# Performance work log

Hardware: AMD Instinct MI355X
Metric: run time of the kernel (lower is better)

The kernel has to match this reference:

```python
import jax, jax.numpy as jnp
import numpy as np

# Module constants (from init_kwargs)
N_BANDS = 15
BW = 129          # uniform bandwidth of every band
HOP = 64
N_FREQ = 1025
EMB = 128
MLP = 512
C = 2             # in_channel (stereo)
REIM = 2          # complex mask -> (real, imag)
OUT = BW * C * REIM   # 516 ; pre-GLU linear outputs 2*OUT
STARTS = np.arange(N_BANDS) * HOP  # band start bins
LN_EPS = 1e-5


def setup_inputs() -> dict:
    key = jax.random.key(0)
    ks = jax.random.split(key, 6)
    B, T = 2, 2048
    q = jax.random.normal(ks[0], (B, N_BANDS, T, EMB), jnp.float32)
    # Per-band LayerNorm affine params
    ln_gamma = jnp.ones((N_BANDS, EMB), jnp.float32)
    ln_beta = jnp.zeros((N_BANDS, EMB), jnp.float32)
    # Per-band hidden Linear (emb -> mlp) and output Linear (mlp -> 2*OUT, then GLU)
    W1 = jax.random.normal(ks[1], (N_BANDS, EMB, MLP), jnp.float32) * (1.0 / np.sqrt(EMB))
    b1 = jax.random.normal(ks[2], (N_BANDS, MLP), jnp.float32) * 0.01
    W2 = jax.random.normal(ks[3], (N_BANDS, MLP, 2 * OUT), jnp.float32) * (1.0 / np.sqrt(MLP))
    b2 = jax.random.normal(ks[4], (N_BANDS, 2 * OUT), jnp.float32) * 0.01
    # Per-band frequency weights (buffers), shape [n_bands, bandwidth]
    freq_weights = jax.random.uniform(ks[5], (N_BANDS, BW), jnp.float32, 0.1, 1.0)
    return {"q": q, "ln_gamma": ln_gamma, "ln_beta": ln_beta,
            "W1": W1, "b1": b1, "W2": W2, "b2": b2,
            "freq_weights": freq_weights}


def reference(q, ln_gamma, ln_beta, W1, b1, W2, b2, freq_weights):
    # q: [B, n_bands, T, emb]
    B, n, T, E = q.shape
    # Per-band LayerNorm over last dim
    mu = jnp.mean(q, axis=-1, keepdims=True)
    var = jnp.mean(jnp.square(q - mu), axis=-1, keepdims=True)
    qn = (q - mu) * jax.lax.rsqrt(var + LN_EPS)
    qn = qn * ln_gamma[None, :, None, :] + ln_beta[None, :, None, :]
    # hidden: Linear + Tanh (batched over bands)
    h = jnp.tanh(jnp.einsum('bnte,nef->bntf', qn, W1) + b1[None, :, None, :])
    # output: Linear + GLU(dim=-1)
    o = jnp.einsum('bntf,nfo->bnto', h, W2) + b2[None, :, None, :]
    a, g = o[..., :OUT], o[..., OUT:]
    m = a * jax.nn.sigmoid(g)                      # [B, n, T, OUT]
    # reshape_output: [B, n, T, C, BW, reim] -> (permute 0,2,3,1 per band) -> [B, C, n, BW, T, reim]
    m = m.reshape(B, n, T, C, BW, REIM)
    m = jnp.transpose(m, (0, 3, 1, 4, 2, 5))       # [B, C, n, BW, T, 2]
    # freq weighting: fw[:, None] broadcast over time
    m = m * freq_weights[None, None, :, :, None, None]
    # Overlapping scatter-add into [B, C, n_freq, T, 2]
    idx = (jnp.asarray(STARTS)[:, None] + jnp.arange(BW)[None, :]).reshape(-1)  # [n*BW]
    masks = jnp.zeros((B, C, N_FREQ, T, REIM), q.dtype)
    masks = masks.at[:, :, idx, :, :].add(m.reshape(B, C, n * BW, T, REIM))
    # Last dim (real, imag) is the real view of the complex mask.
    return masks
```

## Files before the change

kernel.cpp:

```cpp
#include <hip/hip_runtime.h>
#include <math.h>

#define NB    15
#define BWID  129
#define HOP   64
#define NFREQ 1025
#define EMB   128
#define MLP   512
#define OUTC  516
#define O2    1032
#define BATCH 2
#define TLEN  2048
#define REIM  2
#define CCH   2
#define RTOT  (BATCH*NB*TLEN)

typedef _Float16 half8 __attribute__((ext_vector_type(8)));
typedef _Float16 half4 __attribute__((ext_vector_type(4)));
typedef _Float16 half2_ __attribute__((ext_vector_type(2)));
typedef float    floatx4 __attribute__((ext_vector_type(4)));

#define GLOAD_LDS(gsrc, ldst) \
  __builtin_amdgcn_global_load_lds((const __attribute__((address_space(1))) unsigned int*)(gsrc), \
                                   (__attribute__((address_space(3))) unsigned int*)(ldst), 16, 0, 0)

__global__ __launch_bounds__(256) void ln_kernel(const float* __restrict__ q,
                                                 const float* __restrict__ gamma,
                                                 const float* __restrict__ beta,
                                                 _Float16* __restrict__ qn)
{
    int row  = blockIdx.x * 4 + (threadIdx.x >> 6);
    int lane = threadIdx.x & 63;
    int n    = (row / TLEN) % NB;

    const float2* src = (const float2*)(q + (size_t)row * EMB);
    float2 v = src[lane];
    float s  = v.x + v.y;
    float s2 = v.x * v.x + v.y * v.y;
    #pragma unroll
    for (int off = 1; off < 64; off <<= 1) {
        s  += __shfl_xor(s,  off);
        s2 += __shfl_xor(s2, off);
    }
    float mu   = s * (1.0f / EMB);
    float var  = s2 * (1.0f / EMB) - mu * mu;
    float rstd = rsqrtf(var + 1e-5f);

    float2 g2 = ((const float2*)(gamma + n * EMB))[lane];
    float2 b2 = ((const float2*)(beta  + n * EMB))[lane];
    half2_ o;
    o[0] = (_Float16)((v.x - mu) * rstd * g2.x + b2.x);
    o[1] = (_Float16)((v.y - mu) * rstd * g2.y + b2.y);
    ((half2_*)(qn + (size_t)row * EMB))[lane] = o;
}

__global__ __launch_bounds__(256) void transpose_cvt(const float* __restrict__ src,
                                                     _Float16* __restrict__ dst,
                                                     int R, int C)
{
    __shared__ float tile[32][33];
    const int band = blockIdx.z;
    src += (size_t)band * R * C;
    dst += (size_t)band * R * C;
    int tx = threadIdx.x & 31, ty = threadIdx.x >> 5;
    int c0 = blockIdx.x * 32, r0 = blockIdx.y * 32;
    int c = c0 + tx;
    if (c < C) {
        #pragma unroll
        for (int i = 0; i < 4; ++i)
            tile[ty + i * 8][tx] = src[(size_t)(r0 + ty + i * 8) * C + c];
    }
    __syncthreads();
    int cl = threadIdx.x >> 3, rq = (threadIdx.x & 7) * 4;
    int cw = c0 + cl;
    if (cw < C) {
        half4 v;
        #pragma unroll
        for (int j = 0; j < 4; ++j) v[j] = (_Float16)tile[rq + j][cl];
        *(half4*)(dst + (size_t)cw * R + r0 + rq) = v;
    }
}

__global__ __launch_bounds__(256) void gemm1_mfma(const _Float16* __restrict__ qn,
                                                  const _Float16* __restrict__ W1T,
                                                  const float* __restrict__ b1,
                                                  _Float16* __restrict__ h)
{
    __shared__ _Float16 sA[128 * 64];
    __shared__ _Float16 sB[128 * 64];
    const int n   = blockIdx.z;
    const int m0  = blockIdx.y * 128;
    const int n0  = blockIdx.x * 128;
    const int tid = threadIdx.x;
    const int lane = tid & 63;
    const int wave = tid >> 6;
    const int wr = (wave >> 1) * 64;
    const int wc = (wave & 1) * 64;
    const int b = m0 >> 11, t0 = m0 & (TLEN - 1);

    const _Float16* Ab = qn  + ((size_t)(b * NB + n) * TLEN + t0) * EMB;
    const _Float16* Bb = W1T + ((size_t)n * MLP + n0) * EMB;

    floatx4 acc[4][4] = {};

    const int lrow = lane & 15;
    const int q16  = (lane >> 4) << 4;
    const int swz  = (lane & 7) << 4;

    for (int k0 = 0; k0 < EMB; k0 += 64) {
        #pragma unroll
        for (int i = 0; i < 4; ++i) {
            int g = tid + i * 256;
            int r = g >> 3, kb = g & 7;
            int sk = kb ^ (r & 7);
            GLOAD_LDS(Ab + (size_t)r * EMB + k0 + sk * 8, sA + g * 8);
            GLOAD_LDS(Bb + (size_t)r * EMB + k0 + sk * 8, sB + g * 8);
        }
        __syncthreads();
        #pragma unroll
        for (int kk = 0; kk < 2; ++kk) {
            half8 af[4], bf[4];
            #pragma unroll
            for (int m = 0; m < 4; ++m) {
                int r = wr + m * 16 + lrow;
                af[m] = *(const half8*)((const char*)sA + r * 128 + (((kk << 6) | q16) ^ swz));
            }
            #pragma unroll
            for (int nf = 0; nf < 4; ++nf) {
                int r = wc + nf * 16 + lrow;
                bf[nf] = *(const half8*)((const char*)sB + r * 128 + (((kk << 6) | q16) ^ swz));
            }
            #pragma unroll
            for (int m = 0; m < 4; ++m)
                #pragma unroll
                for (int nf = 0; nf < 4; ++nf)
                    acc[m][nf] = __builtin_amdgcn_mfma_f32_16x16x32_f16(af[m], bf[nf], acc[m][nf], 0, 0, 0);
        }
        __syncthreads();
    }

    const int rq = (lane >> 4) * 4;
    _Float16* hb = h + ((size_t)(b * NB + n) * TLEN + t0) * MLP;
    #pragma unroll
    for (int nf = 0; nf < 4; ++nf) {
        int col = n0 + wc + nf * 16 + lrow;
        float bias = b1[n * MLP + col];
        #pragma unroll
        for (int m = 0; m < 4; ++m) {
            int rbase = wr + m * 16 + rq;
            #pragma unroll
            for (int r = 0; r < 4; ++r) {
                float v = tanhf(acc[m][nf][r] + bias);
                hb[(size_t)(rbase + r) * MLP + col] = (_Float16)v;
            }
        }
    }
}

__global__ __launch_bounds__(512) void gemm2_mfma(const _Float16* __restrict__ h,
                                                  const _Float16* __restrict__ W2T,
                                                  const float* __restrict__ b2,
                                                  const float* __restrict__ fw,
                                                  _Float16* __restrict__ mws)
{
    __shared__ _Float16 sA[3 * 256 * 64];
    __shared__ _Float16 sB[3 * 128 * 64];

    const int NWG = 9 * 16 * NB;
    int flat = blockIdx.x;
    int wg   = (flat & 7) * (NWG / 8) + (flat >> 3);
    int bx   = wg % 9;
    int tmp  = wg / 9;
    int by   = tmp & 15;
    int n    = tmp >> 4;

    const int m0  = by * 256;
    const int n0  = bx * 64;
    const int tid = threadIdx.x;
    const int lane = tid & 63;
    const int wave = tid >> 6;
    const int wm = (wave >> 1) * 64;
    const int wc = (wave & 1) * 32;
    const int b = m0 >> 11, t0 = m0 & (TLEN - 1);

    const _Float16* Ab  = h   + ((size_t)(b * NB + n) * TLEN + t0) * MLP;
    const _Float16* W2n = W2T + (size_t)n * O2 * MLP;

    floatx4 accA[4][2] = {};
    floatx4 accG[4][2] = {};

    const int lrow = lane & 15;
    const int q16  = (lane >> 4) << 4;
    const int swz  = (lane & 7) << 4;

    auto stageA2 = [&](int slot, int k0, int i0) {
        #pragma unroll
        for (int i = i0; i < i0 + 2; ++i) {
            int g = tid + i * 512;
            int r = g >> 3;
            int sk = (g & 7) ^ (r & 7);
            GLOAD_LDS(Ab + (size_t)r * MLP + k0 + sk * 8, sA + slot * 16384 + g * 8);
        }
    };
    auto stageBa = [&](int slot, int k0) {
        int g = tid, r = g >> 3;
        int sk = (g & 7) ^ (r & 7);
        int ra = n0 + r; if (ra > OUTC - 1) ra = OUTC - 1;
        GLOAD_LDS(W2n + (size_t)ra * MLP + k0 + sk * 8, sB + slot * 8192 + g * 8);
    };
    auto stageBg = [&](int slot, int k0) {
        int g = tid, r = g >> 3;
        int sk = (g & 7) ^ (r & 7);
        int rg = OUTC + n0 + r; if (rg > O2 - 1) rg = O2 - 1;
        GLOAD_LDS(W2n + (size_t)rg * MLP + k0 + sk * 8, sB + slot * 8192 + 4096 + g * 8);
    };

    stageA2(0, 0, 0);  stageBa(0, 0);
    stageA2(0, 0, 2);  stageBg(0, 0);
    stageA2(1, 64, 0); stageBa(1, 64);
    stageA2(1, 64, 2); stageBg(1, 64);

    for (int kt = 0; kt < 8; ++kt) {
        if (kt < 7) asm volatile("s_waitcnt vmcnt(6)" ::: "memory");
        else        asm volatile("s_waitcnt vmcnt(0)" ::: "memory");
        __builtin_amdgcn_sched_barrier(0);
        __builtin_amdgcn_s_barrier();
        __builtin_amdgcn_sched_barrier(0);

        const int cur = kt % 3;
        const int kt2 = kt + 2;
        const int pre = kt2 % 3;
        const int kp  = kt2 * 64;
        const bool ds = kt2 < 8;
        const _Float16* sAc = sA + cur * 16384;
        const _Float16* sBc = sB + cur * 8192;

        #pragma unroll
        for (int kk = 0; kk < 2; ++kk) {
            half8 af[4], ba[2], bg[2];
            const int koff = (kk << 6) | q16;
            #pragma unroll
            for (int m = 0; m < 4; ++m)
                af[m] = *(const half8*)((const char*)sAc + (wm + m * 16 + lrow) * 128 + (koff ^ swz));
            #pragma unroll
            for (int nf = 0; nf < 2; ++nf) {
                ba[nf] = *(const half8*)((const char*)sBc + (wc + nf * 16 + lrow) * 128 + (koff ^ swz));
                bg[nf] = *(const half8*)((const char*)sBc + 8192 + (wc + nf * 16 + lrow) * 128 + (koff ^ swz));
            }
            if (ds) {
                if (kk == 0) { stageA2(pre, kp, 0); stageBa(pre, kp); }
                else         { stageA2(pre, kp, 2); stageBg(pre, kp); }
            }
            __builtin_amdgcn_sched_barrier(0);
            __builtin_amdgcn_s_barrier();
            asm volatile("s_waitcnt lgkmcnt(0)" ::: "memory");
            __builtin_amdgcn_sched_barrier(0);
            __builtin_amdgcn_s_setprio(1);
            #pragma unroll
            for (int m = 0; m < 4; ++m)
                #pragma unroll
                for (int nf = 0; nf < 2; ++nf) {
                    accA[m][nf] = __builtin_amdgcn_mfma_f32_16x16x32_f16(af[m], ba[nf], accA[m][nf], 0, 0, 0);
                    accG[m][nf] = __builtin_amdgcn_mfma_f32_16x16x32_f16(af[m], bg[nf], accG[m][nf], 0, 0, 0);
                }
            __builtin_amdgcn_s_setprio(0);
            __builtin_amdgcn_sched_barrier(0);
            if (kk == 0) __builtin_amdgcn_s_barrier();
        }
    }

    const int rq = (lane >> 4) * 4;
    const float* b2n = b2 + n * O2;
    #pragma unroll
    for (int nf = 0; nf < 2; ++nf) {
        int c = n0 + wc + nf * 16 + lrow;
        bool valid = c < OUTC;
        int cl = valid ? c : OUTC - 1;
        float biasA = b2n[cl];
        float biasG = b2n[OUTC + cl];
        int rem = cl % 258;
        float w = fw[n * BWID + (rem >> 1)];
        _Float16* mb = mws + ((size_t)((b * NB + n) * OUTC + cl)) * TLEN + t0;
        #pragma unroll
        for (int m = 0; m < 4; ++m) {
            int tb = wm + m * 16 + rq;
            half4 vals;
            #pragma unroll
            for (int r = 0; r < 4; ++r) {
                float a = accA[m][nf][r] + biasA;
                float g = accG[m][nf][r] + biasG;
                vals[r] = (_Float16)(a * w / (1.0f + expf(-g)));
            }
            if (valid) *(half4*)(mb + tb) = vals;
        }
    }
}

__global__ __launch_bounds__(256) void gather_masks(const _Float16* __restrict__ mws,
                                                    float* __restrict__ out)
{
    const int f  = blockIdx.x;
    const int bc = blockIdx.y;
    const int b  = bc >> 1, cc = bc & 1;
    int nlo = (f >= 129) ? ((f - 65) >> 6) : 0;
    int nhi = f >> 6; if (nhi > 14) nhi = 14;
    const int t0 = threadIdx.x * 8;

    float a[8] = {0,0,0,0,0,0,0,0};
    float g[8] = {0,0,0,0,0,0,0,0};
    for (int nn = nlo; nn <= nhi; ++nn) {
        int bw = f - (nn << 6);
        int cbase = cc * 258 + (bw << 1);
        const _Float16* p = mws + ((size_t)((b * NB + nn) * OUTC + cbase)) * TLEN + t0;
        half8 va = *(const half8*)p;
        half8 vg = *(const half8*)(p + TLEN);
        #pragma unroll
        for (int j = 0; j < 8; ++j) { a[j] += (float)va[j]; g[j] += (float)vg[j]; }
    }
    float* ob = out + (((size_t)bc * NFREQ + f) * TLEN + t0) * REIM;
    #pragma unroll
    for (int j = 0; j < 4; ++j) {
        float4 v = make_float4(a[2*j], g[2*j], a[2*j+1], g[2*j+1]);
        *(float4*)(ob + j * 4) = v;
    }
}

extern "C" void kernel_launch(void* const* d_in, const int* in_sizes, int n_in,
                              void* d_out, int out_size, void* d_ws, size_t ws_size,
                              hipStream_t stream) {
    const float* q     = (const float*)d_in[0];
    const float* gamma = (const float*)d_in[1];
    const float* beta  = (const float*)d_in[2];
    const float* W1    = (const float*)d_in[3];
    const float* b1    = (const float*)d_in[4];
    const float* W2    = (const float*)d_in[5];
    const float* b2    = (const float*)d_in[6];
    const float* fw    = (const float*)d_in[7];

    _Float16* hws  = (_Float16*)d_ws;
    _Float16* mws  = hws + (size_t)RTOT * MLP;
    _Float16* qnws = mws + (size_t)BATCH * NB * OUTC * TLEN;
    _Float16* W1T  = qnws + (size_t)RTOT * EMB;
    _Float16* W2T  = qnws;

    ln_kernel<<<RTOT / 4, 256, 0, stream>>>(q, gamma, beta, qnws);
    transpose_cvt<<<dim3(16, 4, NB), 256, 0, stream>>>(W1, W1T, EMB, MLP);
    gemm1_mfma<<<dim3(4, 32, NB), 256, 0, stream>>>(qnws, W1T, b1, hws);
    transpose_cvt<<<dim3(33, 16, NB), 256, 0, stream>>>(W2, W2T, MLP, O2);
    gemm2_mfma<<<9 * 16 * NB, 512, 0, stream>>>(hws, W2T, b2, fw, mws);
    gather_masks<<<dim3(NFREQ, BATCH * CCH), 256, 0, stream>>>(mws, (float*)d_out);
}
```

Measured before the change: 313.5 us.

## Merge weight transposes, widen LayerNorm loads, simplify gemm2 to double buffering

LayerNorm now processes rows with 32 lanes each using float4 loads and half4 stores. The two weight transpose launches are merged into one, with W2T placed in its own workspace region after W1T so it no longer aliases qn. In gemm2, the triple-buffered pipeline with manual vmcnt waits and split barriers is replaced by a double buffer that syncs with __syncthreads. This cuts LDS use and may raise occupancy, but it drops the deeper prefetch and the fine-grained overlap of loads with MFMA work.

```diff
diff --git a/kernel.cpp b/kernel.cpp
--- a/kernel.cpp
+++ b/kernel.cpp
@@ -13,11 +13,10 @@
 #define TLEN  2048
 #define REIM  2
 #define CCH   2
-#define RTOT  (BATCH*NB*TLEN)
+#define RTOT  (BATCH*TLEN*NB)
 
 typedef _Float16 half8 __attribute__((ext_vector_type(8)));
 typedef _Float16 half4 __attribute__((ext_vector_type(4)));
-typedef _Float16 half2_ __attribute__((ext_vector_type(2)));
 typedef float    floatx4 __attribute__((ext_vector_type(4)));
 
 #define GLOAD_LDS(gsrc, ldst) \
@@ -29,16 +28,15 @@
                                                  const float* __restrict__ beta,
                                                  _Float16* __restrict__ qn)
 {
-    int row  = blockIdx.x * 4 + (threadIdx.x >> 6);
-    int lane = threadIdx.x & 63;
-    int n    = (row / TLEN) % NB;
-
-    const float2* src = (const float2*)(q + (size_t)row * EMB);
-    float2 v = src[lane];
-    float s  = v.x + v.y;
-    float s2 = v.x * v.x + v.y * v.y;
+    int row = blockIdx.x * 8 + (threadIdx.x >> 5);
+    int l32 = threadIdx.x & 31;
+    int n   = (row / TLEN) % NB;
+
+    float4 v = ((const float4*)(q + (size_t)row * EMB))[l32];
+    float s  = v.x + v.y + v.z + v.w;
+    float s2 = v.x * v.x + v.y * v.y + v.z * v.z + v.w * v.w;
     #pragma unroll
-    for (int off = 1; off < 64; off <<= 1) {
+    for (int off = 1; off < 32; off <<= 1) {
         s  += __shfl_xor(s,  off);
         s2 += __shfl_xor(s2, off);
     }
@@ -46,24 +44,36 @@
     float var  = s2 * (1.0f / EMB) - mu * mu;
     float rstd = rsqrtf(var + 1e-5f);
 
-    float2 g2 = ((const float2*)(gamma + n * EMB))[lane];
-    float2 b2 = ((const float2*)(beta  + n * EMB))[lane];
-    half2_ o;
-    o[0] = (_Float16)((v.x - mu) * rstd * g2.x + b2.x);
-    o[1] = (_Float16)((v.y - mu) * rstd * g2.y + b2.y);
-    ((half2_*)(qn + (size_t)row * EMB))[lane] = o;
-}
-
-__global__ __launch_bounds__(256) void transpose_cvt(const float* __restrict__ src,
-                                                     _Float16* __restrict__ dst,
-                                                     int R, int C)
+    float4 g4 = ((const float4*)(gamma + n * EMB))[l32];
+    float4 b4 = ((const float4*)(beta  + n * EMB))[l32];
+    half4 o;
+    o[0] = (_Float16)((v.x - mu) * rstd * g4.x + b4.x);
+    o[1] = (_Float16)((v.y - mu) * rstd * g4.y + b4.y);
+    o[2] = (_Float16)((v.z - mu) * rstd * g4.z + b4.z);
+    o[3] = (_Float16)((v.w - mu) * rstd * g4.w + b4.w);
+    ((half4*)(qn + (size_t)row * EMB))[l32] = o;
+}
+
+__global__ __launch_bounds__(256) void transpose_cvt_all(const float* __restrict__ W1,
+                                                         const float* __restrict__ W2,
+                                                         _Float16* __restrict__ W1T,
+                                                         _Float16* __restrict__ W2T)
 {
     __shared__ float tile[32][33];
-    const int band = blockIdx.z;
-    src += (size_t)band * R * C;
-    dst += (size_t)band * R * C;
+    int bid = blockIdx.x;
+    const float* src; _Float16* dst; int R, C, bx, by;
+    if (bid < 960) {
+        int band = bid >> 6; int t = bid & 63; bx = t & 15; by = t >> 4;
+        R = EMB; C = MLP;
+        src = W1 + (size_t)band * R * C; dst = W1T + (size_t)band * R * C;
+    } else {
+        int b2 = bid - 960;
+        int band = b2 / 528; int t = b2 % 528; bx = t % 33; by = t / 33;
+        R = MLP; C = O2;
+        src = W2 + (size_t)band * R * C; dst = W2T + (size_t)band * R * C;
+    }
     int tx = threadIdx.x & 31, ty = threadIdx.x >> 5;
-    int c0 = blockIdx.x * 32, r0 = blockIdx.y * 32;
+    int c0 = bx * 32, r0 = by * 32;
     int c = c0 + tx;
     if (c < C) {
         #pragma unroll
@@ -163,8 +173,8 @@
                                                   const float* __restrict__ fw,
                                                   _Float16* __restrict__ mws)
 {
-    __shared__ _Float16 sA[3 * 256 * 64];
-    __shared__ _Float16 sB[3 * 128 * 64];
+    __shared__ _Float16 sA[2 * 256 * 64];
+    __shared__ _Float16 sB[2 * 128 * 64];
 
     const int NWG = 9 * 16 * NB;
     int flat = blockIdx.x;
@@ -193,48 +203,32 @@
     const int q16  = (lane >> 4) << 4;
     const int swz  = (lane & 7) << 4;
 
-    auto stageA2 = [&](int slot, int k0, int i0) {
-        #pragma unroll
-        for (int i = i0; i < i0 + 2; ++i) {
+    auto stage = [&](int slot, int k0) {
+        #pragma unroll
+        for (int i = 0; i < 4; ++i) {
             int g = tid + i * 512;
             int r = g >> 3;
             int sk = (g & 7) ^ (r & 7);
             GLOAD_LDS(Ab + (size_t)r * MLP + k0 + sk * 8, sA + slot * 16384 + g * 8);
         }
+        {
+            int g = tid, r = g >> 3;
+            int sk = (g & 7) ^ (r & 7);
+            int ra = n0 + r;        if (ra > OUTC - 1) ra = OUTC - 1;
+            int rg = OUTC + n0 + r; if (rg > O2 - 1)   rg = O2 - 1;
+            GLOAD_LDS(W2n + (size_t)ra * MLP + k0 + sk * 8, sB + slot * 8192 + g * 8);
+            GLOAD_LDS(W2n + (size_t)rg * MLP + k0 + sk * 8, sB + slot * 8192 + 4096 + g * 8);
+        }
     };
-    auto stageBa = [&](int slot, int k0) {
-        int g = tid, r = g >> 3;
-        int sk = (g & 7) ^ (r & 7);
-        int ra = n0 + r; if (ra > OUTC - 1) ra = OUTC - 1;
-        GLOAD_LDS(W2n + (size_t)ra * MLP + k0 + sk * 8, sB + slot * 8192 + g * 8);
-    };
-    auto stageBg = [&](int slot, int k0) {
-        int g = tid, r = g >> 3;
-        int sk = (g & 7) ^ (r & 7);
-        int rg = OUTC + n0 + r; if (rg > O2 - 1) rg = O2 - 1;
-        GLOAD_LDS(W2n + (size_t)rg * MLP + k0 + sk * 8, sB + slot * 8192 + 4096 + g * 8);
-    };
-
-    stageA2(0, 0, 0);  stageBa(0, 0);
-    stageA2(0, 0, 2);  stageBg(0, 0);
-    stageA2(1, 64, 0); stageBa(1, 64);
-    stageA2(1, 64, 2); stageBg(1, 64);
+
+    stage(0, 0);
+    __syncthreads();
 
     for (int kt = 0; kt < 8; ++kt) {
-        if (kt < 7) asm volatile("s_waitcnt vmcnt(6)" ::: "memory");
-        else        asm volatile("s_waitcnt vmcnt(0)" ::: "memory");
-        __builtin_amdgcn_sched_barrier(0);
-        __builtin_amdgcn_s_barrier();
-        __builtin_amdgcn_sched_barrier(0);
-
-        const int cur = kt % 3;
-        const int kt2 = kt + 2;
-        const int pre = kt2 % 3;
-        const int kp  = kt2 * 64;
-        const bool ds = kt2 < 8;
+        const int cur = kt & 1;
+        if (kt < 7) stage(cur ^ 1, (kt + 1) * 64);
         const _Float16* sAc = sA + cur * 16384;
         const _Float16* sBc = sB + cur * 8192;
-
         #pragma unroll
         for (int kk = 0; kk < 2; ++kk) {
             half8 af[4], ba[2], bg[2];
@@ -247,14 +241,6 @@
                 ba[nf] = *(const half8*)((const char*)sBc + (wc + nf * 16 + lrow) * 128 + (koff ^ swz));
                 bg[nf] = *(const half8*)((const char*)sBc + 8192 + (wc + nf * 16 + lrow) * 128 + (koff ^ swz));
             }
-            if (ds) {
-                if (kk == 0) { stageA2(pre, kp, 0); stageBa(pre, kp); }
-                else         { stageA2(pre, kp, 2); stageBg(pre, kp); }
-            }
-            __builtin_amdgcn_sched_barrier(0);
-            __builtin_amdgcn_s_barrier();
-            asm volatile("s_waitcnt lgkmcnt(0)" ::: "memory");
-            __builtin_amdgcn_sched_barrier(0);
             __builtin_amdgcn_s_setprio(1);
             #pragma unroll
             for (int m = 0; m < 4; ++m)
@@ -264,9 +250,8 @@
                     accG[m][nf] = __builtin_amdgcn_mfma_f32_16x16x32_f16(af[m], bg[nf], accG[m][nf], 0, 0, 0);
                 }
             __builtin_amdgcn_s_setprio(0);
-            __builtin_amdgcn_sched_barrier(0);
-            if (kk == 0) __builtin_amdgcn_s_barrier();
-        }
+        }
+        __syncthreads();
     }
 
     const int rq = (lane >> 4) * 4;
@@ -341,12 +326,11 @@
     _Float16* mws  = hws + (size_t)RTOT * MLP;
     _Float16* qnws = mws + (size_t)BATCH * NB * OUTC * TLEN;
     _Float16* W1T  = qnws + (size_t)RTOT * EMB;
-    _Float16* W2T  = qnws;
-
-    ln_kernel<<<RTOT / 4, 256, 0, stream>>>(q, gamma, beta, qnws);
-    transpose_cvt<<<dim3(16, 4, NB), 256, 0, stream>>>(W1, W1T, EMB, MLP);
+    _Float16* W2T  = W1T + (size_t)NB * EMB * MLP;
+
+    ln_kernel<<<RTOT / 8, 256, 0, stream>>>(q, gamma, beta, qnws);
+    transpose_cvt_all<<<960 + 528 * NB, 256, 0, stream>>>(W1, W2, W1T, W2T);
     gemm1_mfma<<<dim3(4, 32, NB), 256, 0, stream>>>(qnws, W1T, b1, hws);
-    transpose_cvt<<<dim3(33, 16, NB), 256, 0, stream>>>(W2, W2T, MLP, O2);
     gemm2_mfma<<<9 * 16 * NB, 512, 0, stream>>>(hws, W2T, b2, fw, mws);
     gather_masks<<<dim3(NFREQ, BATCH * CCH), 256, 0, stream>>>(mws, (float*)d_out);
 }
```

Result: slower. 321.9 us (+2.7%).
